# Kernel tuning notes

Hardware: AMD Instinct MI355X
Metric: run time of the kernel (lower is better)

Reference implementation:

```python
import jax, jax.numpy as jnp
import numpy as np

N_NODES = 100000
N_EDGES = 800000
N_LAYERS = 6
GATE_TYPES = 29
H = 256        # hidden dim
INTER = 256    # inter dim
EDGE_F = 3     # (src_idx, dst_idx, reversed) edge features


def setup_inputs() -> dict:
    key = jax.random.key(0)
    ks = jax.random.split(key, 16)
    gate_type = jax.random.randint(ks[0], (N_NODES,), 0, GATE_TYPES)
    src = jax.random.randint(ks[1], (N_EDGES,), 0, N_NODES)
    dst = jax.random.randint(ks[2], (N_EDGES,), 0, N_NODES)
    w = jax.random.uniform(ks[3], (N_EDGES, EDGE_F), dtype=jnp.float32)
    s = 0.05
    emb = jax.random.normal(ks[4], (GATE_TYPES, H), dtype=jnp.float32) * s
    # QConv per layer: linear1 (no bias): [INTER, H+3]; linear2: [H, H+INTER] + bias
    W1 = jax.random.normal(ks[5], (N_LAYERS, INTER, H + EDGE_F), dtype=jnp.float32) * s
    W2 = jax.random.normal(ks[6], (N_LAYERS, H, H + INTER), dtype=jnp.float32) * s
    b2 = jax.random.normal(ks[7], (N_LAYERS, H), dtype=jnp.float32) * s
    # MLP head 256->256->1
    Wh1 = jax.random.normal(ks[8], (H, H), dtype=jnp.float32) * s
    bh1 = jax.random.normal(ks[9], (H,), dtype=jnp.float32) * s
    Wh2 = jax.random.normal(ks[10], (1, H), dtype=jnp.float32) * s
    bh2 = jax.random.normal(ks[11], (1,), dtype=jnp.float32) * s
    return {"gate_type": gate_type, "src": src, "dst": dst, "w": w,
            "emb": emb, "W1": W1, "W2": W2, "b2": b2,
            "Wh1": Wh1, "bh1": bh1, "Wh2": Wh2, "bh2": bh2}


def reference(gate_type, src, dst, w, emb, W1, W2, b2, Wh1, bh1, Wh2, bh2):
    n = gate_type.shape[0]
    h = emb[gate_type]                                   # [N, H]
    deg = jax.ops.segment_sum(jnp.ones((src.shape[0],), h.dtype), dst, num_segments=n)
    inv_deg = (1.0 / jnp.maximum(deg, 1.0))[:, None]      # mean over mailbox; 0-deg nodes -> h_N = 0
    for l in range(W1.shape[0]):
        m = jnp.concatenate([h[src], w], axis=1)          # [E, H+3] gather
        tmp = jax.nn.leaky_relu(m @ W1[l].T, 0.01)        # [E, INTER]
        h_N = jax.ops.segment_sum(tmp, dst, num_segments=n) * inv_deg  # scatter-mean [N, INTER]
        h = jax.nn.relu(jnp.concatenate([h, h_N], axis=1) @ W2[l].T + b2[l])
    x = jax.nn.relu(h @ Wh1.T + bh1)                      # [N, H]
    return x @ Wh2.T + bh2                                # [N, 1]
```

## Files before the change

### kernel.cpp

```cpp
#include <hip/hip_runtime.h>

#define H 256
#define NLAYERS 6
typedef unsigned int uint32;
typedef unsigned short u16;

typedef __bf16 bf16;
typedef bf16 bf16x8 __attribute__((ext_vector_type(8)));
typedef float f32x4 __attribute__((ext_vector_type(4)));

__device__ __forceinline__ float bf2f(u16 h) {
    return __uint_as_float(((uint32)h) << 16);
}
__device__ __forceinline__ u16 f2bf(float f) {
    uint32 u = __float_as_uint(f);
    u = u + 0x7FFFu + ((u >> 16) & 1u);
    return (u16)(u >> 16);
}

__device__ __forceinline__ void glds16(const void* src, const char* ldsdst) {
    __builtin_amdgcn_global_load_lds(
        (const __attribute__((address_space(1))) void*)src,
        (__attribute__((address_space(3))) void*)ldsdst, 16, 0, 0);
}


__global__ __launch_bounds__(256)
void count_kernel(const int* __restrict__ dst, int* __restrict__ deg, int E) {
    int e = blockIdx.x * 256 + threadIdx.x;
    if (e < E) atomicAdd(&deg[dst[e]], 1);
}

__global__ __launch_bounds__(256)
void invd_kernel(const int* __restrict__ deg, float* __restrict__ invd, int N) {
    int n = blockIdx.x * 256 + threadIdx.x;
    if (n < N) invd[n] = 1.f / fmaxf((float)deg[n], 1.f);
}

__global__ __launch_bounds__(256)
void scan1_kernel(const int* __restrict__ deg, int* __restrict__ bsum, int N) {
    __shared__ int s[256];
    int t = threadIdx.x;
    int i = blockIdx.x * 256 + t;
    s[t] = (i < N) ? deg[i] : 0;
    __syncthreads();
    for (int off = 128; off; off >>= 1) {
        if (t < off) s[t] += s[t + off];
        __syncthreads();
    }
    if (t == 0) bsum[blockIdx.x] = s[0];
}

__global__ __launch_bounds__(512)
void scan2_kernel(int* __restrict__ bsum, int nb) {
    __shared__ int s[512];
    int t = threadIdx.x;
    int v = (t < nb) ? bsum[t] : 0;
    s[t] = v;
    __syncthreads();
    for (int off = 1; off < 512; off <<= 1) {
        int x = (t >= off) ? s[t - off] : 0;
        __syncthreads();
        s[t] += x;
        __syncthreads();
    }
    if (t < nb) bsum[t] = s[t] - v;
}

__global__ __launch_bounds__(256)
void scan3_kernel(const int* __restrict__ deg, const int* __restrict__ bsum,
                  int* __restrict__ rowptr, int N, int E) {
    __shared__ int s[256];
    int t = threadIdx.x;
    int i = blockIdx.x * 256 + t;
    int v = (i < N) ? deg[i] : 0;
    s[t] = v;
    __syncthreads();
    for (int off = 1; off < 256; off <<= 1) {
        int x = (t >= off) ? s[t - off] : 0;
        __syncthreads();
        s[t] += x;
        __syncthreads();
    }
    if (i < N) rowptr[i] = s[t] - v + bsum[blockIdx.x];
    if (i == 0) rowptr[N] = E;
}

__global__ __launch_bounds__(256)
void scatter_kernel(const int* __restrict__ src, const int* __restrict__ dst,
                    const float* __restrict__ w, const int* __restrict__ rowptr,
                    int* __restrict__ cursor, int* __restrict__ srcS,
                    float* __restrict__ wS, int E) {
    int e = blockIdx.x * 256 + threadIdx.x;
    if (e >= E) return;
    int d = dst[e];
    int p = rowptr[d] + atomicAdd(&cursor[d], 1);
    srcS[p] = src[e];
    wS[(size_t)p * 3 + 0] = w[(size_t)e * 3 + 0];
    wS[(size_t)p * 3 + 1] = w[(size_t)e * 3 + 1];
    wS[(size_t)p * 3 + 2] = w[(size_t)e * 3 + 2];
}


__global__ __launch_bounds__(256)
void wsplit_kernel(const float* __restrict__ W1, const float* __restrict__ W2,
                   const float* __restrict__ Wh1,
                   u16* __restrict__ W1hi, u16* __restrict__ W1lo,
                   u16* __restrict__ W2hi, u16* __restrict__ W2lo,
                   u16* __restrict__ Wh1hi, u16* __restrict__ Wh1lo)
{
    int i = blockIdx.x * 256 + threadIdx.x;
    float v; u16* ph; u16* pl; int o;
    if (i < 393216) {
        int l = i >> 16, rem = i & 65535, r = rem >> 8, k = rem & 255;
        v = W1[(size_t)l * 66304 + (size_t)r * 259 + k];
        ph = W1hi; pl = W1lo; o = i;
    } else if (i < 1179648) {
        int j = i - 393216;
        v = W2[j];
        ph = W2hi; pl = W2lo; o = j;
    } else if (i < 1245184) {
        int j = i - 1179648;
        v = Wh1[j];
        ph = Wh1hi; pl = Wh1lo; o = j;
    } else return;
    u16 hi = f2bf(v);
    ph[o] = hi;
    pl[o] = f2bf(v - bf2f(hi));
}


__global__ __launch_bounds__(256)
void emb_split_kernel(const int* __restrict__ gt, const float* __restrict__ emb,
                      u16* __restrict__ hHi, u16* __restrict__ hLo, int N) {
    size_t idx = (size_t)blockIdx.x * 256 + threadIdx.x;
    if (idx >= (size_t)N * 256) return;
    int n = (int)(idx >> 8), c = (int)(idx & 255);
    float v = emb[(size_t)gt[n] * 256 + c];
    u16 hi = f2bf(v);
    hHi[idx] = hi;
    hLo[idx] = f2bf(v - bf2f(hi));
}


#define LDS_AHI 0
#define LDS_ALO 4096
#define LDS_WHI 8192
#define LDS_WLO 24576

template<bool MAIN>
__device__ __forceinline__ void do_compute(const char* lds, const int* aoff,
                                           const int* woff, f32x4 (&acc)[4][4]) {
    bf16x8 ah[4], al[4];
    #pragma unroll
    for (int mi = 0; mi < 4; ++mi) {
        ah[mi] = *(const bf16x8*)(lds + LDS_AHI + aoff[mi]);
        if (MAIN) al[mi] = *(const bf16x8*)(lds + LDS_ALO + aoff[mi]);
    }
    #pragma unroll
    for (int nj = 0; nj < 4; ++nj) {
        bf16x8 wh = *(const bf16x8*)(lds + LDS_WHI + woff[nj]);
        bf16x8 wl = *(const bf16x8*)(lds + LDS_WLO + woff[nj]);
        #pragma unroll
        for (int mi = 0; mi < 4; ++mi) {
            acc[mi][nj] = __builtin_amdgcn_mfma_f32_16x16x32_bf16(ah[mi], wh, acc[mi][nj], 0, 0, 0);
            acc[mi][nj] = __builtin_amdgcn_mfma_f32_16x16x32_bf16(ah[mi], wl, acc[mi][nj], 0, 0, 0);
            if (MAIN)
                acc[mi][nj] = __builtin_amdgcn_mfma_f32_16x16x32_bf16(al[mi], wh, acc[mi][nj], 0, 0, 0);
        }
    }
}

template<int KTOT, bool BIASRELU, bool WLO>
__global__ __launch_bounds__(256)
void mfma_gemm_kernel(const u16* __restrict__ Ahi_, const u16* __restrict__ Alo_,
                      const u16* __restrict__ A2_,
                      const u16* __restrict__ Whi_, const u16* __restrict__ Wlo_,
                      const float* __restrict__ bias,
                      u16* __restrict__ Chi, u16* __restrict__ Clo, int M)
{
    __shared__ __align__(128) char lds[40960];
    const int tid = threadIdx.x;
    const int wv = tid >> 6;
    const int lane = tid & 63;
    const int m0 = blockIdx.x * 64;
    const int lrow = lane & 15, koct = lane >> 4;

    int aoff[4], woff[4];
    #pragma unroll
    for (int mi = 0; mi < 4; ++mi) {
        int r = mi * 16 + lrow;
        aoff[mi] = r * 64 + ((koct ^ (r & 3)) << 4);
    }
    #pragma unroll
    for (int nj = 0; nj < 4; ++nj) {
        int r = wv * 64 + nj * 16 + lrow;
        woff[nj] = r * 64 + ((koct ^ (r & 3)) << 4);
    }

    const int arow = tid >> 2;
    const int acs = (tid & 3) ^ (arow & 3);
    const long agrow = (long)((m0 + arow < M) ? (m0 + arow) : (M - 1));
    const char* Asrc_hi = (const char*)Ahi_ + agrow * 512 + acs * 16;
    const char* Asrc_lo = (const char*)Alo_ + agrow * 512 + acs * 16;
    const char* Asrc_2  = (const char*)A2_  + agrow * 512 + acs * 16;

    f32x4 acc[4][4] = {};

    for (int k0 = 0; k0 < 256; k0 += 32) {
        glds16(Asrc_hi + k0 * 2, lds + LDS_AHI + wv * 1024);
        glds16(Asrc_lo + k0 * 2, lds + LDS_ALO + wv * 1024);
        #pragma unroll
        for (int rr = 0; rr < 4; ++rr) {
            int f = rr * 256 + tid;
            int wr = f >> 2;
            int wcs = (f & 3) ^ (wr & 3);
            glds16((const char*)Whi_ + (long)wr * (KTOT * 2) + k0 * 2 + wcs * 16,
                   lds + LDS_WHI + rr * 4096 + wv * 1024);
            glds16((const char*)Wlo_ + (long)wr * (KTOT * 2) + k0 * 2 + wcs * 16,
                   lds + LDS_WLO + rr * 4096 + wv * 1024);
        }
        __syncthreads();
        do_compute<true>(lds, aoff, woff, acc);
        __syncthreads();
    }
    if (KTOT > 256) {
        for (int k0 = 256; k0 < KTOT; k0 += 32) {
            glds16(Asrc_2 + (k0 - 256) * 2, lds + LDS_AHI + wv * 1024);
            #pragma unroll
            for (int rr = 0; rr < 4; ++rr) {
                int f = rr * 256 + tid;
                int wr = f >> 2;
                int wcs = (f & 3) ^ (wr & 3);
                glds16((const char*)Whi_ + (long)wr * (KTOT * 2) + k0 * 2 + wcs * 16,
                       lds + LDS_WHI + rr * 4096 + wv * 1024);
                glds16((const char*)Wlo_ + (long)wr * (KTOT * 2) + k0 * 2 + wcs * 16,
                       lds + LDS_WLO + rr * 4096 + wv * 1024);
            }
            __syncthreads();
            do_compute<false>(lds, aoff, woff, acc);
            __syncthreads();
        }
    }

    float bv[4] = {0.f, 0.f, 0.f, 0.f};
    if (BIASRELU) {
        #pragma unroll
        for (int nj = 0; nj < 4; ++nj) bv[nj] = bias[wv * 64 + nj * 16 + lrow];
    }
    #pragma unroll
    for (int mi = 0; mi < 4; ++mi) {
        #pragma unroll
        for (int r = 0; r < 4; ++r) {
            int row = m0 + mi * 16 + koct * 4 + r;
            if (row >= M) continue;
            #pragma unroll
            for (int nj = 0; nj < 4; ++nj) {
                float v = acc[mi][nj][r];
                if (BIASRELU) v = fmaxf(v + bv[nj], 0.f);
                size_t o = (size_t)row * 256 + wv * 64 + nj * 16 + lrow;
                u16 hi = f2bf(v);
                Chi[o] = hi;
                if (WLO) Clo[o] = f2bf(v - bf2f(hi));
            }
        }
    }
}


__global__ __launch_bounds__(256)
void edge_agg_kernel(const int* __restrict__ rowptr, const int* __restrict__ srcS,
                     const float* __restrict__ wS, const u16* __restrict__ T,
                     const float* __restrict__ W1l, const float* __restrict__ invd,
                     u16* __restrict__ hN, int N) {
    int n = blockIdx.x * 4 + (threadIdx.x >> 6);
    int lane = threadIdx.x & 63;
    if (n >= N) return;
    int col0 = lane * 4;
    float c0[4], c1[4], c2[4];
    #pragma unroll
    for (int q = 0; q < 4; ++q) {
        const float* wp = W1l + (size_t)(col0 + q) * 259 + 256;
        c0[q] = wp[0]; c1[q] = wp[1]; c2[q] = wp[2];
    }
    float acc[4] = {0.f, 0.f, 0.f, 0.f};
    int e0 = rowptr[n], e1 = rowptr[n + 1];
    for (int e = e0; e < e1; ++e) {
        int s = srcS[e];
        float w0 = wS[(size_t)e * 3 + 0];
        float w1 = wS[(size_t)e * 3 + 1];
        float w2 = wS[(size_t)e * 3 + 2];
        ushort4 tv = *(const ushort4*)&T[(size_t)s * H + col0];
        float v_[4] = {bf2f(tv.x), bf2f(tv.y), bf2f(tv.z), bf2f(tv.w)};
        #pragma unroll
        for (int q = 0; q < 4; ++q) {
            float x = v_[q] + w0 * c0[q] + w1 * c1[q] + w2 * c2[q];
            acc[q] += (x > 0.f) ? x : 0.01f * x;
        }
    }
    float sc = invd[n];
    ushort4 o;
    o.x = f2bf(acc[0] * sc); o.y = f2bf(acc[1] * sc);
    o.z = f2bf(acc[2] * sc); o.w = f2bf(acc[3] * sc);
    *(ushort4*)&hN[(size_t)n * H + col0] = o;
}


__global__ __launch_bounds__(256)
void head_out_kernel(const u16* __restrict__ xhi, const u16* __restrict__ xlo,
                     const float* __restrict__ wh2,
                     const float* __restrict__ bh2, float* __restrict__ out, int N) {
    int n = blockIdx.x * 4 + (threadIdx.x >> 6);
    int lane = threadIdx.x & 63;
    if (n >= N) return;
    ushort4 hv = ((const ushort4*)(xhi + (size_t)n * H))[lane];
    ushort4 lv = ((const ushort4*)(xlo + (size_t)n * H))[lane];
    float4 wv = ((const float4*)wh2)[lane];
    float x0 = bf2f(hv.x) + bf2f(lv.x);
    float x1 = bf2f(hv.y) + bf2f(lv.y);
    float x2 = bf2f(hv.z) + bf2f(lv.z);
    float x3 = bf2f(hv.w) + bf2f(lv.w);
    float sum = x0 * wv.x + x1 * wv.y + x2 * wv.z + x3 * wv.w;
    #pragma unroll
    for (int off = 32; off; off >>= 1) sum += __shfl_xor(sum, off);
    if (lane == 0) out[n] = sum + bh2[0];
}


extern "C" void kernel_launch(void* const* d_in, const int* in_sizes, int n_in,
                              void* d_out, int out_size, void* d_ws, size_t ws_size,
                              hipStream_t stream) {
    const int*   gate_type = (const int*)d_in[0];
    const int*   src  = (const int*)d_in[1];
    const int*   dst  = (const int*)d_in[2];
    const float* w    = (const float*)d_in[3];
    const float* emb  = (const float*)d_in[4];
    const float* W1   = (const float*)d_in[5];
    const float* W2   = (const float*)d_in[6];
    const float* b2   = (const float*)d_in[7];
    const float* Wh1  = (const float*)d_in[8];
    const float* bh1  = (const float*)d_in[9];
    const float* Wh2  = (const float*)d_in[10];
    const float* bh2  = (const float*)d_in[11];
    float* out = (float*)d_out;

    const int N = in_sizes[0];
    const int E = in_sizes[1];

    char* p = (char*)d_ws;
    auto alloc = [&](size_t bytes) -> char* {
        char* r = p;
        p += (bytes + 1023) & ~(size_t)1023;
        return r;
    };
    u16*   hHi   = (u16*)  alloc((size_t)N * H * 2);
    u16*   hLo   = (u16*)  alloc((size_t)N * H * 2);
    u16*   tBuf  = (u16*)  alloc((size_t)N * H * 2);
    u16*   hNBuf = (u16*)  alloc((size_t)N * H * 2);
    int*   srcS  = (int*)  alloc((size_t)E * 4);
    float* wS    = (float*)alloc((size_t)E * 3 * 4);
    int*   rowptr= (int*)  alloc((size_t)(N + 1) * 4);
    int*   cursor= (int*)  alloc((size_t)N * 4);
    int*   bsum  = (int*)  alloc(4096);
    float* invd  = (float*)alloc((size_t)N * 4);
    u16*   W1hi  = (u16*)  alloc(6u * 256 * 256 * 2);
    u16*   W1lo  = (u16*)  alloc(6u * 256 * 256 * 2);
    u16*   W2hi  = (u16*)  alloc(6u * 256 * 512 * 2);
    u16*   W2lo  = (u16*)  alloc(6u * 256 * 512 * 2);
    u16*   Wh1hi = (u16*)  alloc(256u * 256 * 2);
    u16*   Wh1lo = (u16*)  alloc(256u * 256 * 2);

    const int nb1 = (N + 255) / 256;

    hipMemsetAsync(cursor, 0, (size_t)N * 4, stream);
    count_kernel<<<(E + 255) / 256, 256, 0, stream>>>(dst, cursor, E);
    invd_kernel<<<nb1, 256, 0, stream>>>(cursor, invd, N);
    scan1_kernel<<<nb1, 256, 0, stream>>>(cursor, bsum, N);
    scan2_kernel<<<1, 512, 0, stream>>>(bsum, nb1);
    scan3_kernel<<<nb1, 256, 0, stream>>>(cursor, bsum, rowptr, N, E);
    hipMemsetAsync(cursor, 0, (size_t)N * 4, stream);
    scatter_kernel<<<(E + 255) / 256, 256, 0, stream>>>(src, dst, w, rowptr, cursor, srcS, wS, E);

    wsplit_kernel<<<4864, 256, 0, stream>>>(W1, W2, Wh1, W1hi, W1lo, W2hi, W2lo, Wh1hi, Wh1lo);
    emb_split_kernel<<<N, 256, 0, stream>>>(gate_type, emb, hHi, hLo, N);

    const int gm = (N + 63) / 64;
    for (int l = 0; l < NLAYERS; ++l) {
        const float* W1l = W1 + (size_t)l * 256 * 259;
        mfma_gemm_kernel<256, false, false><<<gm, 256, 0, stream>>>(
            hHi, hLo, nullptr, W1hi + (size_t)l * 65536, W1lo + (size_t)l * 65536,
            nullptr, tBuf, nullptr, N);
        edge_agg_kernel<<<(N + 3) / 4, 256, 0, stream>>>(rowptr, srcS, wS, tBuf, W1l, invd, hNBuf, N);
        mfma_gemm_kernel<512, true, true><<<gm, 256, 0, stream>>>(
            hHi, hLo, hNBuf, W2hi + (size_t)l * 131072, W2lo + (size_t)l * 131072,
            b2 + (size_t)l * 256, hHi, hLo, N);
    }
    mfma_gemm_kernel<256, true, true><<<gm, 256, 0, stream>>>(
        hHi, hLo, nullptr, Wh1hi, Wh1lo, bh1, hHi, hLo, N);
    head_out_kernel<<<(N + 3) / 4, 256, 0, stream>>>(hHi, hLo, Wh2, bh2, out, N);
}
```

Baseline: 2.208 ms.

## Vectorize edge aggregation, pad edge weights, transpose MFMA for vector stores

The edge aggregation kernel now splits each node's edges between the two half-waves, with each lane handling 8 columns through 16-byte gathers. Two edges are processed per iteration and the halves are combined with a cross-lane shuffle. Edge weights are padded to float4, and the per-column W1 edge coefficients are pre-extracted into a contiguous buffer so they can be loaded with vector reads. The MFMA operands are swapped so each lane holds 4 consecutive output columns, which lets the GEMM epilogue write ushort4 stores instead of scalar 2-byte stores. In exchange, the padded edge weights use more memory and the edge loop carries more registers.

```diff
diff --git a/kernel.cpp b/kernel.cpp
--- a/kernel.cpp
+++ b/kernel.cpp
@@ -8,6 +8,7 @@
 typedef __bf16 bf16;
 typedef bf16 bf16x8 __attribute__((ext_vector_type(8)));
 typedef float f32x4 __attribute__((ext_vector_type(4)));
+typedef u16 u16x8 __attribute__((ext_vector_type(8)));
 
 __device__ __forceinline__ float bf2f(u16 h) {
     return __uint_as_float(((uint32)h) << 16);
@@ -96,9 +97,12 @@
     int d = dst[e];
     int p = rowptr[d] + atomicAdd(&cursor[d], 1);
     srcS[p] = src[e];
-    wS[(size_t)p * 3 + 0] = w[(size_t)e * 3 + 0];
-    wS[(size_t)p * 3 + 1] = w[(size_t)e * 3 + 1];
-    wS[(size_t)p * 3 + 2] = w[(size_t)e * 3 + 2];
+    float4 wq;
+    wq.x = w[(size_t)e * 3 + 0];
+    wq.y = w[(size_t)e * 3 + 1];
+    wq.z = w[(size_t)e * 3 + 2];
+    wq.w = 0.f;
+    *(float4*)&wS[(size_t)p * 4] = wq;
 }
 
 
@@ -129,6 +133,17 @@
     pl[o] = f2bf(v - bf2f(hi));
 }
 
+__global__ void extract_kernel(const float* __restrict__ W1, float* __restrict__ ccAll)
+{
+    int l = blockIdx.x;
+    int i = threadIdx.x;
+    const float* W1l = W1 + (size_t)l * 66304;
+    float* cc = ccAll + (size_t)l * 768;
+    #pragma unroll
+    for (int j = 0; j < 3; ++j)
+        cc[j * 256 + i] = W1l[(size_t)i * 259 + 256 + j];
+}
+
 
 __global__ __launch_bounds__(256)
 void emb_split_kernel(const int* __restrict__ gt, const float* __restrict__ emb,
@@ -163,10 +178,10 @@
         bf16x8 wl = *(const bf16x8*)(lds + LDS_WLO + woff[nj]);
         #pragma unroll
         for (int mi = 0; mi < 4; ++mi) {
-            acc[mi][nj] = __builtin_amdgcn_mfma_f32_16x16x32_bf16(ah[mi], wh, acc[mi][nj], 0, 0, 0);
-            acc[mi][nj] = __builtin_amdgcn_mfma_f32_16x16x32_bf16(ah[mi], wl, acc[mi][nj], 0, 0, 0);
+            acc[mi][nj] = __builtin_amdgcn_mfma_f32_16x16x32_bf16(wh, ah[mi], acc[mi][nj], 0, 0, 0);
+            acc[mi][nj] = __builtin_amdgcn_mfma_f32_16x16x32_bf16(wl, ah[mi], acc[mi][nj], 0, 0, 0);
             if (MAIN)
-                acc[mi][nj] = __builtin_amdgcn_mfma_f32_16x16x32_bf16(al[mi], wh, acc[mi][nj], 0, 0, 0);
+                acc[mi][nj] = __builtin_amdgcn_mfma_f32_16x16x32_bf16(wh, al[mi], acc[mi][nj], 0, 0, 0);
         }
     }
 }
@@ -243,25 +258,37 @@
         }
     }
 
-    float bv[4] = {0.f, 0.f, 0.f, 0.f};
+    float4 bv[4];
     if (BIASRELU) {
         #pragma unroll
-        for (int nj = 0; nj < 4; ++nj) bv[nj] = bias[wv * 64 + nj * 16 + lrow];
+        for (int nj = 0; nj < 4; ++nj)
+            bv[nj] = *(const float4*)&bias[wv * 64 + nj * 16 + koct * 4];
     }
     #pragma unroll
     for (int mi = 0; mi < 4; ++mi) {
-        #pragma unroll
-        for (int r = 0; r < 4; ++r) {
-            int row = m0 + mi * 16 + koct * 4 + r;
-            if (row >= M) continue;
-            #pragma unroll
-            for (int nj = 0; nj < 4; ++nj) {
-                float v = acc[mi][nj][r];
-                if (BIASRELU) v = fmaxf(v + bv[nj], 0.f);
-                size_t o = (size_t)row * 256 + wv * 64 + nj * 16 + lrow;
-                u16 hi = f2bf(v);
-                Chi[o] = hi;
-                if (WLO) Clo[o] = f2bf(v - bf2f(hi));
+        int row = m0 + mi * 16 + lrow;
+        if (row >= M) continue;
+        #pragma unroll
+        for (int nj = 0; nj < 4; ++nj) {
+            f32x4 v = acc[mi][nj];
+            if (BIASRELU) {
+                v[0] = fmaxf(v[0] + bv[nj].x, 0.f);
+                v[1] = fmaxf(v[1] + bv[nj].y, 0.f);
+                v[2] = fmaxf(v[2] + bv[nj].z, 0.f);
+                v[3] = fmaxf(v[3] + bv[nj].w, 0.f);
+            }
+            size_t o = (size_t)row * 256 + wv * 64 + nj * 16 + koct * 4;
+            ushort4 ohi;
+            ohi.x = f2bf(v[0]); ohi.y = f2bf(v[1]);
+            ohi.z = f2bf(v[2]); ohi.w = f2bf(v[3]);
+            *(ushort4*)&Chi[o] = ohi;
+            if (WLO) {
+                ushort4 olo;
+                olo.x = f2bf(v[0] - bf2f(ohi.x));
+                olo.y = f2bf(v[1] - bf2f(ohi.y));
+                olo.z = f2bf(v[2] - bf2f(ohi.z));
+                olo.w = f2bf(v[3] - bf2f(ohi.w));
+                *(ushort4*)&Clo[o] = olo;
             }
         }
     }
@@ -271,38 +298,62 @@
 __global__ __launch_bounds__(256)
 void edge_agg_kernel(const int* __restrict__ rowptr, const int* __restrict__ srcS,
                      const float* __restrict__ wS, const u16* __restrict__ T,
-                     const float* __restrict__ W1l, const float* __restrict__ invd,
+                     const float* __restrict__ cc, const float* __restrict__ invd,
                      u16* __restrict__ hN, int N) {
     int n = blockIdx.x * 4 + (threadIdx.x >> 6);
     int lane = threadIdx.x & 63;
     if (n >= N) return;
-    int col0 = lane * 4;
-    float c0[4], c1[4], c2[4];
-    #pragma unroll
-    for (int q = 0; q < 4; ++q) {
-        const float* wp = W1l + (size_t)(col0 + q) * 259 + 256;
-        c0[q] = wp[0]; c1[q] = wp[1]; c2[q] = wp[2];
-    }
-    float acc[4] = {0.f, 0.f, 0.f, 0.f};
-    int e0 = rowptr[n], e1 = rowptr[n + 1];
-    for (int e = e0; e < e1; ++e) {
-        int s = srcS[e];
-        float w0 = wS[(size_t)e * 3 + 0];
-        float w1 = wS[(size_t)e * 3 + 1];
-        float w2 = wS[(size_t)e * 3 + 2];
-        ushort4 tv = *(const ushort4*)&T[(size_t)s * H + col0];
-        float v_[4] = {bf2f(tv.x), bf2f(tv.y), bf2f(tv.z), bf2f(tv.w)};
-        #pragma unroll
-        for (int q = 0; q < 4; ++q) {
-            float x = v_[q] + w0 * c0[q] + w1 * c1[q] + w2 * c2[q];
+    const int half = lane >> 5;
+    const int c32 = lane & 31;
+    const int col0 = c32 * 8;
+
+    float c0[8], c1[8], c2[8];
+    #pragma unroll
+    for (int j = 0; j < 3; ++j) {
+        float4 lo4 = *(const float4*)&cc[j * 256 + col0];
+        float4 hi4 = *(const float4*)&cc[j * 256 + col0 + 4];
+        float* cj = (j == 0) ? c0 : (j == 1) ? c1 : c2;
+        cj[0] = lo4.x; cj[1] = lo4.y; cj[2] = lo4.z; cj[3] = lo4.w;
+        cj[4] = hi4.x; cj[5] = hi4.y; cj[6] = hi4.z; cj[7] = hi4.w;
+    }
+
+    float acc[8] = {};
+    const int e0 = rowptr[n], e1 = rowptr[n + 1];
+    int e = e0 + half;
+    for (; e + 2 < e1; e += 4) {
+        int s0 = srcS[e];
+        int s1 = srcS[e + 2];
+        float4 wa = *(const float4*)&wS[(size_t)e * 4];
+        float4 wb = *(const float4*)&wS[(size_t)(e + 2) * 4];
+        u16x8 t0 = *(const u16x8*)&T[(size_t)s0 * 256 + col0];
+        u16x8 t1 = *(const u16x8*)&T[(size_t)s1 * 256 + col0];
+        #pragma unroll
+        for (int q = 0; q < 8; ++q) {
+            float x = fmaf(wa.x, c0[q], fmaf(wa.y, c1[q], fmaf(wa.z, c2[q], bf2f(t0[q]))));
             acc[q] += (x > 0.f) ? x : 0.01f * x;
-        }
-    }
-    float sc = invd[n];
-    ushort4 o;
-    o.x = f2bf(acc[0] * sc); o.y = f2bf(acc[1] * sc);
-    o.z = f2bf(acc[2] * sc); o.w = f2bf(acc[3] * sc);
-    *(ushort4*)&hN[(size_t)n * H + col0] = o;
+            float y = fmaf(wb.x, c0[q], fmaf(wb.y, c1[q], fmaf(wb.z, c2[q], bf2f(t1[q]))));
+            acc[q] += (y > 0.f) ? y : 0.01f * y;
+        }
+    }
+    for (; e < e1; e += 2) {
+        int s0 = srcS[e];
+        float4 wa = *(const float4*)&wS[(size_t)e * 4];
+        u16x8 t0 = *(const u16x8*)&T[(size_t)s0 * 256 + col0];
+        #pragma unroll
+        for (int q = 0; q < 8; ++q) {
+            float x = fmaf(wa.x, c0[q], fmaf(wa.y, c1[q], fmaf(wa.z, c2[q], bf2f(t0[q]))));
+            acc[q] += (x > 0.f) ? x : 0.01f * x;
+        }
+    }
+    #pragma unroll
+    for (int q = 0; q < 8; ++q) acc[q] += __shfl_xor(acc[q], 32);
+    if (half == 0) {
+        float sc = invd[n];
+        u16x8 o;
+        #pragma unroll
+        for (int q = 0; q < 8; ++q) o[q] = f2bf(acc[q] * sc);
+        *(u16x8*)&hN[(size_t)n * 256 + col0] = o;
+    }
 }
 
 
@@ -358,11 +409,12 @@
     u16*   tBuf  = (u16*)  alloc((size_t)N * H * 2);
     u16*   hNBuf = (u16*)  alloc((size_t)N * H * 2);
     int*   srcS  = (int*)  alloc((size_t)E * 4);
-    float* wS    = (float*)alloc((size_t)E * 3 * 4);
+    float* wS    = (float*)alloc((size_t)E * 4 * 4);
     int*   rowptr= (int*)  alloc((size_t)(N + 1) * 4);
     int*   cursor= (int*)  alloc((size_t)N * 4);
     int*   bsum  = (int*)  alloc(4096);
     float* invd  = (float*)alloc((size_t)N * 4);
+    float* ccAll = (float*)alloc(6u * 768 * 4);
     u16*   W1hi  = (u16*)  alloc(6u * 256 * 256 * 2);
     u16*   W1lo  = (u16*)  alloc(6u * 256 * 256 * 2);
     u16*   W2hi  = (u16*)  alloc(6u * 256 * 512 * 2);
@@ -382,15 +434,16 @@
     scatter_kernel<<<(E + 255) / 256, 256, 0, stream>>>(src, dst, w, rowptr, cursor, srcS, wS, E);
 
     wsplit_kernel<<<4864, 256, 0, stream>>>(W1, W2, Wh1, W1hi, W1lo, W2hi, W2lo, Wh1hi, Wh1lo);
+    extract_kernel<<<6, 256, 0, stream>>>(W1, ccAll);
     emb_split_kernel<<<N, 256, 0, stream>>>(gate_type, emb, hHi, hLo, N);
 
     const int gm = (N + 63) / 64;
     for (int l = 0; l < NLAYERS; ++l) {
-        const float* W1l = W1 + (size_t)l * 256 * 259;
         mfma_gemm_kernel<256, false, false><<<gm, 256, 0, stream>>>(
             hHi, hLo, nullptr, W1hi + (size_t)l * 65536, W1lo + (size_t)l * 65536,
             nullptr, tBuf, nullptr, N);
-        edge_agg_kernel<<<(N + 3) / 4, 256, 0, stream>>>(rowptr, srcS, wS, tBuf, W1l, invd, hNBuf, N);
+        edge_agg_kernel<<<(N + 3) / 4, 256, 0, stream>>>(
+            rowptr, srcS, wS, tBuf, ccAll + (size_t)l * 768, invd, hNBuf, N);
         mfma_gemm_kernel<512, true, true><<<gm, 256, 0, stream>>>(
             hHi, hLo, hNBuf, W2hi + (size_t)l * 131072, W2lo + (size_t)l * 131072,
             b2 + (size_t)l * 256, hHi, hLo, N);
```

Measured after the change: 1.885 ms. 14.6% less time.
